# Kernel optimization log

Hardware: AMD Instinct MI355X
Metric: run time of the kernel (lower is better)

## Reference

```python
import jax, jax.numpy as jnp
import numpy as np

BN_EPS = 1e-5
# regular 3x3 kernel grid offsets: row0 = dy, row1 = dx, kernel positions in row-major order
REG = jnp.array([[-1, -1, -1, 0, 0, 0, 1, 1, 1],
                 [-1,  0,  1, -1, 0, 1, -1, 0, 1]], dtype=jnp.float32)


def conv3x3(x, w, b):
    y = jax.lax.conv_general_dilated(x, w, window_strides=(1, 1),
                                     padding=((1, 1), (1, 1)),
                                     dimension_numbers=('NCHW', 'OIHW', 'NCHW'))
    return y + b[None, :, None, None]


def deform_conv3x3(x, dy, dx, w):
    # x: [N,C,H,W]; dy,dx: [N,9,H,W] per-kernel-tap offsets; w: [O,C,3,3]
    N, C, H, W = x.shape
    K = 9
    ky = jnp.repeat(jnp.arange(3), 3)   # [0,0,0,1,1,1,2,2,2]
    kx = jnp.tile(jnp.arange(3), 3)     # [0,1,2,0,1,2,0,1,2]
    # sampling positions: p = p_out - pad + k*dilation + offset (stride=1, pad=dil=1)
    py = dy + (jnp.arange(H) - 1)[None, None, :, None] + ky[None, :, None, None].astype(x.dtype)
    px = dx + (jnp.arange(W) - 1)[None, None, None, :] + kx[None, :, None, None].astype(x.dtype)
    y0 = jnp.floor(py)
    x0 = jnp.floor(px)
    wy = py - y0  # bilinear weights
    wx = px - x0
    y0i = y0.astype(jnp.int32)
    x0i = x0.astype(jnp.int32)
    nidx = jnp.arange(N)[:, None, None, None]

    def gather(yi, xi):
        valid = ((yi >= 0) & (yi < H) & (xi >= 0) & (xi < W)).astype(x.dtype)
        v = x[nidx, :, jnp.clip(yi, 0, H - 1), jnp.clip(xi, 0, W - 1)]  # [N,K,H,W,C]
        return v * valid[..., None]

    sampled = (gather(y0i,     x0i)     * ((1 - wy) * (1 - wx))[..., None]
             + gather(y0i,     x0i + 1) * ((1 - wy) * wx)[..., None]
             + gather(y0i + 1, x0i)     * (wy * (1 - wx))[..., None]
             + gather(y0i + 1, x0i + 1) * (wy * wx)[..., None])  # [N,K,H,W,C]
    O = w.shape[0]
    return jnp.einsum('nkhwc,ock->nohw', sampled, w.reshape(O, C, K))


def setup_inputs() -> dict:
    key = jax.random.key(0)
    ks = jax.random.split(key, 12)
    N, C, H, W = 2, 256, 96, 96
    O = 256
    sc = 1.0 / np.sqrt(C * 9)
    return {
        'x': jax.random.normal(ks[0], (N, C, H, W), jnp.float32),
        'mask_attention': jax.random.normal(ks[1], (N, C, H, W), jnp.float32),
        'w_tm': jax.random.normal(ks[2], (4, C, 3, 3), jnp.float32) * sc,
        'b_tm': jax.random.normal(ks[3], (4,), jnp.float32) * 0.01,
        'w_tr': jax.random.normal(ks[4], (2, C, 3, 3), jnp.float32) * sc,
        'b_tr': jax.random.normal(ks[5], (2,), jnp.float32) * 0.01,
        'w_deform': jax.random.normal(ks[6], (O, C, 3, 3), jnp.float32) * sc,
        'bn_gamma': jnp.ones((O,), jnp.float32),
        'bn_beta': jnp.zeros((O,), jnp.float32),
        'bn_mean': jax.random.normal(ks[7], (O,), jnp.float32) * 0.01,
        'bn_var': jax.random.uniform(ks[8], (O,), jnp.float32, 0.5, 1.5),
    }


def reference(x, mask_attention, w_tm, b_tm, w_tr, b_tr, w_deform,
              bn_gamma, bn_beta, bn_mean, bn_var):
    # mask_attention is overwritten by x in the original forward; ignored.
    N, C, H, W = x.shape
    tm = conv3x3(x, w_tm, b_tm)                       # [N,4,H,W]
    T = tm.transpose(0, 2, 3, 1).reshape(N, H, W, 2, 2)
    off = jnp.einsum('nhwij,jk->nhwik', T, REG) - REG  # [N,H,W,2,9], (T-I)@REG
    tr = conv3x3(x, w_tr, b_tr)                        # [N,2,H,W]
    off = off + tr.transpose(0, 2, 3, 1)[..., None]    # broadcast translation to all 9 taps
    dy = off[..., 0, :].transpose(0, 3, 1, 2)          # [N,9,H,W]
    dx = off[..., 1, :].transpose(0, 3, 1, 2)
    out = deform_conv3x3(x, dy, dx, w_deform)          # [N,O,H,W]
    inv = jax.lax.rsqrt(bn_var + BN_EPS)
    out = (out - bn_mean[None, :, None, None]) * (inv * bn_gamma)[None, :, None, None] \
          + bn_beta[None, :, None, None]
    return jax.nn.relu(out + x)
```

## Files before the change

kernel.cpp:

```cpp
#include <hip/hip_runtime.h>
#include <stdint.h>

#define H_ 96
#define W_ 96
#define C_ 256
#define O_ 256
#define N_ 2
#define HW_ (H_*W_)
#define M_ (N_*HW_)
#define GK 2304

typedef __bf16 bf16x8 __attribute__((ext_vector_type(8)));
typedef float f32x4 __attribute__((ext_vector_type(4)));
typedef float f32x2 __attribute__((ext_vector_type(2)));
typedef unsigned short us4 __attribute__((ext_vector_type(4)));
typedef unsigned short us8 __attribute__((ext_vector_type(8)));

__device__ __forceinline__ unsigned short f2bf(float f) {
  union { float f; unsigned int u; } v; v.f = f;
  unsigned int u = v.u;
  return (unsigned short)((u + 0x7fffu + ((u >> 16) & 1u)) >> 16);
}
__device__ __forceinline__ float bf2f(unsigned short h) {
  union { unsigned int u; float f; } v; v.u = ((unsigned int)h) << 16;
  return v.f;
}
__device__ __forceinline__ f32x2 bfpair(unsigned int a) {
  union { unsigned int u; float f; } lo, hi;
  lo.u = a << 16;
  hi.u = a & 0xffff0000u;
  f32x2 r; r[0] = lo.f; r[1] = hi.f;
  return r;
}

__global__ __launch_bounds__(256) void k_pre(const float* __restrict__ x,
                                             const float* __restrict__ w_df,
                                             const float* __restrict__ w_tm,
                                             const float* __restrict__ w_tr,
                                             unsigned short* __restrict__ xt,
                                             unsigned short* __restrict__ wfrag,
                                             unsigned short* __restrict__ w6p) {
  const int b = blockIdx.x;
  const int tid = threadIdx.x;
  if (b < 288) {
    __shared__ unsigned short tile[128][130];
    const int pt = b % 72;
    const int ch = (b / 72) & 1;
    const int n  = b / 144;
    const int p0 = pt * 128, c0 = ch * 128;
    const float* xp = x + (size_t)n * C_ * HW_;
    unsigned short* xtp = xt + (size_t)n * C_ * HW_;
    const int tx = tid & 31, ty = tid >> 5;
#pragma unroll
    for (int pass = 0; pass < 16; pass++) {
      const int c = pass * 8 + ty;
      const f32x4 v = *(const f32x4*)(xp + (size_t)(c0 + c) * HW_ + p0 + tx * 4);
#pragma unroll
      for (int i = 0; i < 4; i++) tile[tx * 4 + i][c] = f2bf(v[i]);
    }
    __syncthreads();
    const int wave = tid >> 6, lane = tid & 63;
    const int l32 = lane & 31, ph = lane >> 5;
#pragma unroll
    for (int pass = 0; pass < 16; pass++) {
      const int p = pass * 8 + wave * 2 + ph;
      us4 v;
#pragma unroll
      for (int i = 0; i < 4; i++) v[i] = tile[p][l32 * 4 + i];
      *(us4*)(xtp + (size_t)(p0 + p) * C_ + c0 + l32 * 4) = v;
    }
  } else if (b < 576) {
    const int base = (b - 288) * 2048 + tid * 8;
    const int l  = (base >> 3) & 63;
    const int g  = (base >> 9) & 15;
    const int ks = (base >> 13) & 7;
    const int t  = base >> 16;
    const int o  = g * 16 + (l & 15);
    const int c  = ks * 32 + (l >> 4) * 8;
    us8 res;
#pragma unroll
    for (int j = 0; j < 8; j++) res[j] = f2bf(w_df[(size_t)(o * 256 + c + j) * 9 + t]);
    *(us8*)(wfrag + base) = res;
  } else {
    int idx = (b - 576) * 256 + tid;
    int t = idx >> 12;
    int r = idx & 4095;
    int j = r >> 8;
    int c = r & 255;
    float v = 0.f;
    if (j < 4) v = w_tm[(size_t)(j * C_ + c) * 9 + t];
    else if (j < 6) v = w_tr[(size_t)((j - 4) * C_ + c) * 9 + t];
    w6p[idx] = f2bf(v);
  }
}

__global__ __launch_bounds__(512, 4) void k_fused(const unsigned short* __restrict__ xt,
                                                  const unsigned short* __restrict__ Wfrag,
                                                  const unsigned short* __restrict__ w6p,
                                                  const float* __restrict__ b_tm,
                                                  const float* __restrict__ b_tr,
                                                  const float* __restrict__ xres,
                                                  const float* __restrict__ gamma,
                                                  const float* __restrict__ beta,
                                                  const float* __restrict__ mean,
                                                  const float* __restrict__ var,
                                                  float* __restrict__ out) {
  __shared__ unsigned short As[2][32 * 256] __attribute__((aligned(16)));
  __shared__ float sred[8][16][8];
  __shared__ float coords_s[32][9][2];
  const int tid = threadIdx.x;
  const int wave = tid >> 6, lane = tid & 63;
  const int row = lane & 15, quad = lane >> 4;
  const int bm = (blockIdx.x & 7) * 72 + (blockIdx.x >> 3);
  const int m0 = bm * 32;
  const int n = m0 / HW_;
  const int sr = tid >> 4;
  const int cg = tid & 15;

  {
    const int hw0 = m0 - n * HW_;
    const int h = hw0 / W_;
    const int w0 = hw0 - h * W_;
    const int rh = wave >> 2;
    const int cq = (wave & 3) * 64;
    f32x4 oacc = {0.f, 0.f, 0.f, 0.f};
    const bf16x8 zero8 = {};
#pragma unroll
    for (int t = 0; t < 9; t++) {
      const int ty = t / 3, tx = t % 3;
      const int y = h + ty - 1;
      if (y < 0 || y >= H_) continue;
      const int xx = w0 + rh * 16 + row + tx - 1;
      const bool valid = (xx >= 0) && (xx < W_);
      const int xc = min(max(xx, 0), W_ - 1);
      const unsigned short* arow =
          xt + (size_t)((n * H_ + y) * W_ + xc) * C_ + cq + quad * 8;
      const unsigned short* brow =
          w6p + (size_t)(t * 16 + row) * C_ + cq + quad * 8;
#pragma unroll
      for (int ks = 0; ks < 2; ks++) {
        bf16x8 av = *(const bf16x8*)(const void*)(arow + ks * 32);
        if (!valid) av = zero8;
        bf16x8 bv = *(const bf16x8*)(const void*)(brow + ks * 32);
        oacc = __builtin_amdgcn_mfma_f32_16x16x32_bf16(av, bv, oacc, 0, 0, 0);
      }
    }
    if (row < 6) {
#pragma unroll
      for (int r = 0; r < 4; r++) sred[wave][quad * 4 + r][row] = oacc[r];
    }
  }
  __syncthreads();
  if (wave < 2 && lane < 16) {
    const int rg = wave * 16 + lane;
    const int hwm = m0 + rg - n * HW_;
    const int h = hwm / W_, w = hwm - h * W_;
    float a[6];
#pragma unroll
    for (int j = 0; j < 6; j++)
      a[j] = sred[wave * 4 + 0][lane][j] + sred[wave * 4 + 1][lane][j] +
             sred[wave * 4 + 2][lane][j] + sred[wave * 4 + 3][lane][j];
    const float tm0 = a[0] + b_tm[0];
    const float tm1 = a[1] + b_tm[1];
    const float tm2 = a[2] + b_tm[2];
    const float tm3 = a[3] + b_tm[3];
    const float tr0 = a[4] + b_tr[0];
    const float tr1 = a[5] + b_tr[1];
#pragma unroll
    for (int t = 0; t < 9; t++) {
      const float ry = (float)(t / 3) - 1.f;
      const float rx = (float)(t % 3) - 1.f;
      coords_s[rg][t][0] = (float)h + tr0 + tm0 * ry + tm1 * rx;
      coords_s[rg][t][1] = (float)w + tr1 + tm2 * ry + tm3 * rx;
    }
  }
  __syncthreads();

  f32x4 acc0[2] = {}, acc1[2] = {};
  float cw[4];
  int cb[4];
  us8 u0[4], u1[4];

#define PREP1(TAP)                                                             \
  {                                                                            \
    const float py = coords_s[sr][TAP][0];                                     \
    const float px = coords_s[sr][TAP][1];                                     \
    const float fy = floorf(py), fx = floorf(px);                              \
    const float wy = py - fy, wx = px - fx;                                    \
    const int y0 = (int)fy, x0 = (int)fx;                                      \
    const int y1 = y0 + 1, x1 = x0 + 1;                                        \
    const float vy0 = (y0 >= 0 && y0 < H_) ? 1.f : 0.f;                        \
    const float vy1 = (y1 >= 0 && y1 < H_) ? 1.f : 0.f;                        \
    const float vx0 = (x0 >= 0 && x0 < W_) ? 1.f : 0.f;                        \
    const float vx1 = (x1 >= 0 && x1 < W_) ? 1.f : 0.f;                        \
    cw[0] = (1.f - wy) * (1.f - wx) * vy0 * vx0;                               \
    cw[1] = (1.f - wy) * wx * vy0 * vx1;                                       \
    cw[2] = wy * (1.f - wx) * vy1 * vx0;                                       \
    cw[3] = wy * wx * vy1 * vx1;                                               \
    const int cy0 = min(max(y0, 0), H_ - 1), cy1 = min(max(y1, 0), H_ - 1);    \
    const int cx0 = min(max(x0, 0), W_ - 1), cx1 = min(max(x1, 0), W_ - 1);    \
    cb[0] = ((n * H_ + cy0) * W_ + cx0) * C_;                                  \
    cb[1] = ((n * H_ + cy0) * W_ + cx1) * C_;                                  \
    cb[2] = ((n * H_ + cy1) * W_ + cx0) * C_;                                  \
    cb[3] = ((n * H_ + cy1) * W_ + cx1) * C_;                                  \
  }

#define LOADC1()                                                               \
  {                                                                            \
    const int cc = cg * 16;                                                    \
    u0[0] = *(const us8*)(xt + cb[0] + cc); u1[0] = *(const us8*)(xt + cb[0] + cc + 8); \
    u0[1] = *(const us8*)(xt + cb[1] + cc); u1[1] = *(const us8*)(xt + cb[1] + cc + 8); \
    u0[2] = *(const us8*)(xt + cb[2] + cc); u1[2] = *(const us8*)(xt + cb[2] + cc + 8); \
    u0[3] = *(const us8*)(xt + cb[3] + cc); u1[3] = *(const us8*)(xt + cb[3] + cc + 8); \
  }

#define LERP8V(DST, U)                                                         \
  {                                                                            \
    const unsigned int* a0 = (const unsigned int*)&U[0];                       \
    const unsigned int* a1 = (const unsigned int*)&U[1];                       \
    const unsigned int* a2 = (const unsigned int*)&U[2];                       \
    const unsigned int* a3 = (const unsigned int*)&U[3];                       \
    _Pragma("unroll")                                                          \
    for (int p = 0; p < 4; p++) {                                              \
      f32x2 acc = bfpair(a0[p]) * cw[0] + bfpair(a1[p]) * cw[1] +              \
                  bfpair(a2[p]) * cw[2] + bfpair(a3[p]) * cw[3];               \
      DST[p * 2]     = (__bf16)acc[0];                                         \
      DST[p * 2 + 1] = (__bf16)acc[1];                                         \
    }                                                                          \
  }

  PREP1(0);
  LOADC1();

  for (int tap = 0; tap < 9; tap++) {
    unsigned short* __restrict__ asb = As[tap & 1];
    {
      const int q0 = cg * 2, q1 = cg * 2 + 1;
      const int s0 = (q0 & 24) | ((q0 ^ sr) & 7);
      const int s1 = (q1 & 24) | ((q1 ^ sr) & 7);
      bf16x8 r0, r1;
      LERP8V(r0, u0);
      LERP8V(r1, u1);
      *(bf16x8*)(void*)&asb[sr * 256 + s0 * 8] = r0;
      *(bf16x8*)(void*)&asb[sr * 256 + s1 * 8] = r1;
    }

    const unsigned short* wfTap =
        Wfrag + (size_t)(tap * 8) * 8192 + wave * 1024 + lane * 8;
    bf16x8 bv[2];
#pragma unroll
    for (int ot = 0; ot < 2; ot++) bv[ot] = *(const bf16x8*)(const void*)(wfTap + ot * 512);

    __syncthreads();

    if (tap < 8) {
      PREP1(tap + 1);
      LOADC1();
    }

#pragma unroll
    for (int ks = 0; ks < 8; ks++) {
      const int q = ks * 4 + quad;
      const int slot = (q & 24) | ((q ^ row) & 7);
      const bf16x8 av0 = *(const bf16x8*)(const void*)&asb[row * 256 + slot * 8];
      const bf16x8 av1 = *(const bf16x8*)(const void*)&asb[(row + 16) * 256 + slot * 8];
      bf16x8 bn[2];
      if (ks < 7) {
        const unsigned short* wfn = wfTap + (size_t)(ks + 1) * 8192;
#pragma unroll
        for (int ot = 0; ot < 2; ot++) bn[ot] = *(const bf16x8*)(const void*)(wfn + ot * 512);
      }
#pragma unroll
      for (int ot = 0; ot < 2; ot++)
        acc0[ot] = __builtin_amdgcn_mfma_f32_16x16x32_bf16(av0, bv[ot], acc0[ot], 0, 0, 0);
#pragma unroll
      for (int ot = 0; ot < 2; ot++)
        acc1[ot] = __builtin_amdgcn_mfma_f32_16x16x32_bf16(av1, bv[ot], acc1[ot], 0, 0, 0);
      if (ks < 7) {
#pragma unroll
        for (int ot = 0; ot < 2; ot++) bv[ot] = bn[ot];
      }
    }
  }

  const int hwb = m0 - n * HW_ + quad * 4;
#pragma unroll
  for (int ot = 0; ot < 2; ot++) {
    const int o = wave * 32 + ot * 16 + row;
    const float sc = rsqrtf(var[o] + 1e-5f) * gamma[o];
    const float bi = beta[o] - mean[o] * sc;
    const size_t ob0 = (size_t)(n * O_ + o) * HW_ + hwb;
    f32x4 rv = *(const f32x4*)(xres + ob0);
    f32x4 ov;
#pragma unroll
    for (int r = 0; r < 4; r++) ov[r] = fmaxf(acc0[ot][r] * sc + bi + rv[r], 0.f);
    *(f32x4*)(out + ob0) = ov;
    const size_t ob1 = ob0 + 16;
    rv = *(const f32x4*)(xres + ob1);
#pragma unroll
    for (int r = 0; r < 4; r++) ov[r] = fmaxf(acc1[ot][r] * sc + bi + rv[r], 0.f);
    *(f32x4*)(out + ob1) = ov;
  }
}

extern "C" void kernel_launch(void* const* d_in, const int* in_sizes, int n_in,
                              void* d_out, int out_size, void* d_ws, size_t ws_size,
                              hipStream_t stream) {
  const float* x     = (const float*)d_in[0];
  const float* w_tm  = (const float*)d_in[2];
  const float* b_tm  = (const float*)d_in[3];
  const float* w_tr  = (const float*)d_in[4];
  const float* b_tr  = (const float*)d_in[5];
  const float* w_df  = (const float*)d_in[6];
  const float* gamma = (const float*)d_in[7];
  const float* beta  = (const float*)d_in[8];
  const float* mean  = (const float*)d_in[9];
  const float* var   = (const float*)d_in[10];
  float* out = (float*)d_out;

  char* ws = (char*)d_ws;
  unsigned short* xt    = (unsigned short*)(ws);
  unsigned short* wfrag = (unsigned short*)(ws + 9437184);
  unsigned short* w6p   = (unsigned short*)(ws + 9437184 + 1179648);

  k_pre<<<720, 256, 0, stream>>>(x, w_df, w_tm, w_tr, xt, wfrag, w6p);
  k_fused<<<576, 512, 0, stream>>>(xt, wfrag, w6p, b_tm, b_tr, x,
                                   gamma, beta, mean, var, out);
}
```

Measured before the change: 177.1 us.

## Split output channels across two blocks per pixel tile to double grid size

The fused kernel now assigns each block half of the 256 output channels (bo selects the half), so the grid doubles to 1152 blocks and each wave holds one accumulator pair instead of two. Occupancy hint rises to 8 blocks per CU. The pre-pass transpose also uses smaller 64-pixel tiles with more blocks. The trade-off is that offset prediction and bilinear sampling of the A tile are now computed twice per pixel tile, once in each of the two blocks.

Result: slower. 228.2 us (+28.8%).

```diff
diff --git a/kernel.cpp b/kernel.cpp
--- a/kernel.cpp
+++ b/kernel.cpp
@@ -42,35 +42,34 @@
                                              unsigned short* __restrict__ w6p) {
   const int b = blockIdx.x;
   const int tid = threadIdx.x;
-  if (b < 288) {
-    __shared__ unsigned short tile[128][130];
-    const int pt = b % 72;
-    const int ch = (b / 72) & 1;
-    const int n  = b / 144;
-    const int p0 = pt * 128, c0 = ch * 128;
+  if (b < 576) {
+    __shared__ unsigned short tile[64][130];
+    const int pt = b % 144;
+    const int ch = (b / 144) & 1;
+    const int n  = b / 288;
+    const int p0 = pt * 64, c0 = ch * 128;
     const float* xp = x + (size_t)n * C_ * HW_;
     unsigned short* xtp = xt + (size_t)n * C_ * HW_;
-    const int tx = tid & 31, ty = tid >> 5;
-#pragma unroll
-    for (int pass = 0; pass < 16; pass++) {
-      const int c = pass * 8 + ty;
+    const int tx = tid & 15, ty = tid >> 4;
+#pragma unroll
+    for (int pass = 0; pass < 8; pass++) {
+      const int c = pass * 16 + ty;
       const f32x4 v = *(const f32x4*)(xp + (size_t)(c0 + c) * HW_ + p0 + tx * 4);
 #pragma unroll
       for (int i = 0; i < 4; i++) tile[tx * 4 + i][c] = f2bf(v[i]);
     }
     __syncthreads();
-    const int wave = tid >> 6, lane = tid & 63;
-    const int l32 = lane & 31, ph = lane >> 5;
-#pragma unroll
-    for (int pass = 0; pass < 16; pass++) {
-      const int p = pass * 8 + wave * 2 + ph;
+    const int l32 = tid & 31, pr = tid >> 5;
+#pragma unroll
+    for (int pass = 0; pass < 8; pass++) {
+      const int p = pass * 8 + pr;
       us4 v;
 #pragma unroll
       for (int i = 0; i < 4; i++) v[i] = tile[p][l32 * 4 + i];
       *(us4*)(xtp + (size_t)(p0 + p) * C_ + c0 + l32 * 4) = v;
     }
-  } else if (b < 576) {
-    const int base = (b - 288) * 2048 + tid * 8;
+  } else if (b < 864) {
+    const int base = (b - 576) * 2048 + tid * 8;
     const int l  = (base >> 3) & 63;
     const int g  = (base >> 9) & 15;
     const int ks = (base >> 13) & 7;
@@ -82,7 +81,7 @@
     for (int j = 0; j < 8; j++) res[j] = f2bf(w_df[(size_t)(o * 256 + c + j) * 9 + t]);
     *(us8*)(wfrag + base) = res;
   } else {
-    int idx = (b - 576) * 256 + tid;
+    int idx = (b - 864) * 256 + tid;
     int t = idx >> 12;
     int r = idx & 4095;
     int j = r >> 8;
@@ -94,7 +93,7 @@
   }
 }
 
-__global__ __launch_bounds__(512, 4) void k_fused(const unsigned short* __restrict__ xt,
+__global__ __launch_bounds__(512, 8) void k_fused(const unsigned short* __restrict__ xt,
                                                   const unsigned short* __restrict__ Wfrag,
                                                   const unsigned short* __restrict__ w6p,
                                                   const float* __restrict__ b_tm,
@@ -111,7 +110,9 @@
   const int tid = threadIdx.x;
   const int wave = tid >> 6, lane = tid & 63;
   const int row = lane & 15, quad = lane >> 4;
-  const int bm = (blockIdx.x & 7) * 72 + (blockIdx.x >> 3);
+  const int slot = (blockIdx.x & 7) * 144 + (blockIdx.x >> 3);
+  const int bm = slot >> 1;
+  const int bo = slot & 1;
   const int m0 = bm * 32;
   const int n = m0 / HW_;
   const int sr = tid >> 4;
@@ -176,7 +177,7 @@
   }
   __syncthreads();
 
-  f32x4 acc0[2] = {}, acc1[2] = {};
+  f32x4 acc0 = {}, acc1 = {};
   float cw[4];
   int cb[4];
   us8 u0[4], u1[4];
@@ -234,6 +235,11 @@
 
   for (int tap = 0; tap < 9; tap++) {
     unsigned short* __restrict__ asb = As[tap & 1];
+
+    const unsigned short* wfTap =
+        Wfrag + (size_t)tap * 65536 + (bo * 8 + wave) * 512 + lane * 8;
+    bf16x8 bv = *(const bf16x8*)(const void*)(wfTap);
+
     {
       const int q0 = cg * 2, q1 = cg * 2 + 1;
       const int s0 = (q0 & 24) | ((q0 ^ sr) & 7);
@@ -245,12 +251,6 @@
       *(bf16x8*)(void*)&asb[sr * 256 + s1 * 8] = r1;
     }
 
-    const unsigned short* wfTap =
-        Wfrag + (size_t)(tap * 8) * 8192 + wave * 1024 + lane * 8;
-    bf16x8 bv[2];
-#pragma unroll
-    for (int ot = 0; ot < 2; ot++) bv[ot] = *(const bf16x8*)(const void*)(wfTap + ot * 512);
-
     __syncthreads();
 
     if (tap < 8) {
@@ -264,41 +264,29 @@
       const int slot = (q & 24) | ((q ^ row) & 7);
       const bf16x8 av0 = *(const bf16x8*)(const void*)&asb[row * 256 + slot * 8];
       const bf16x8 av1 = *(const bf16x8*)(const void*)&asb[(row + 16) * 256 + slot * 8];
-      bf16x8 bn[2];
-      if (ks < 7) {
-        const unsigned short* wfn = wfTap + (size_t)(ks + 1) * 8192;
-#pragma unroll
-        for (int ot = 0; ot < 2; ot++) bn[ot] = *(const bf16x8*)(const void*)(wfn + ot * 512);
-      }
-#pragma unroll
-      for (int ot = 0; ot < 2; ot++)
-        acc0[ot] = __builtin_amdgcn_mfma_f32_16x16x32_bf16(av0, bv[ot], acc0[ot], 0, 0, 0);
-#pragma unroll
-      for (int ot = 0; ot < 2; ot++)
-        acc1[ot] = __builtin_amdgcn_mfma_f32_16x16x32_bf16(av1, bv[ot], acc1[ot], 0, 0, 0);
-      if (ks < 7) {
-#pragma unroll
-        for (int ot = 0; ot < 2; ot++) bv[ot] = bn[ot];
-      }
+      bf16x8 bn;
+      if (ks < 7) bn = *(const bf16x8*)(const void*)(wfTap + (size_t)(ks + 1) * 8192);
+      acc0 = __builtin_amdgcn_mfma_f32_16x16x32_bf16(av0, bv, acc0, 0, 0, 0);
+      acc1 = __builtin_amdgcn_mfma_f32_16x16x32_bf16(av1, bv, acc1, 0, 0, 0);
+      if (ks < 7) bv = bn;
     }
   }
 
   const int hwb = m0 - n * HW_ + quad * 4;
-#pragma unroll
-  for (int ot = 0; ot < 2; ot++) {
-    const int o = wave * 32 + ot * 16 + row;
+  {
+    const int o = bo * 128 + wave * 16 + row;
     const float sc = rsqrtf(var[o] + 1e-5f) * gamma[o];
     const float bi = beta[o] - mean[o] * sc;
     const size_t ob0 = (size_t)(n * O_ + o) * HW_ + hwb;
     f32x4 rv = *(const f32x4*)(xres + ob0);
     f32x4 ov;
 #pragma unroll
-    for (int r = 0; r < 4; r++) ov[r] = fmaxf(acc0[ot][r] * sc + bi + rv[r], 0.f);
+    for (int r = 0; r < 4; r++) ov[r] = fmaxf(acc0[r] * sc + bi + rv[r], 0.f);
     *(f32x4*)(out + ob0) = ov;
     const size_t ob1 = ob0 + 16;
     rv = *(const f32x4*)(xres + ob1);
 #pragma unroll
-    for (int r = 0; r < 4; r++) ov[r] = fmaxf(acc1[ot][r] * sc + bi + rv[r], 0.f);
+    for (int r = 0; r < 4; r++) ov[r] = fmaxf(acc1[r] * sc + bi + rv[r], 0.f);
     *(f32x4*)(out + ob1) = ov;
   }
 }
@@ -323,7 +311,7 @@
   unsigned short* wfrag = (unsigned short*)(ws + 9437184);
   unsigned short* w6p   = (unsigned short*)(ws + 9437184 + 1179648);
 
-  k_pre<<<720, 256, 0, stream>>>(x, w_df, w_tm, w_tr, xt, wfrag, w6p);
-  k_fused<<<576, 512, 0, stream>>>(xt, wfrag, w6p, b_tm, b_tr, x,
-                                   gamma, beta, mean, var, out);
-}
+  k_pre<<<1008, 256, 0, stream>>>(x, w_df, w_tm, w_tr, xt, wfrag, w6p);
+  k_fused<<<1152, 512, 0, stream>>>(xt, wfrag, w6p, b_tm, b_tr, x,
+                                    gamma, beta, mean, var, out);
+}
```
